# Performance work log

Hardware: AMD Instinct MI355X
Metric: run time of the kernel (lower is better)

The kernel has to match this reference:

```python
import jax, jax.numpy as jnp
import numpy as np

S = 64          # image_size / sdf cube side / embed dim
P = 4           # frame & sdf patch size
NC = 4          # number_of_couples
HP = 8          # num_heads
E = 32          # embedding_middle_attention
FC = 4          # final_number_of_channels
G = S // P      # 16 patches per side
N_FR = G * G * NC      # 1024 frame tokens
N_SDF = G ** 3         # 4096 sdf tokens
N = N_FR + N_SDF       # 5120 total tokens
NB = N // S            # 80 blocks


def setup_inputs() -> dict:
    key = jax.random.key(0)
    ks = jax.random.split(key, 12)
    s = 0.05  # keep attention logits numerically sane
    return {
        "cond1": jax.random.normal(ks[0], (1, 1, S, S, S), jnp.float32),
        "cond2": jax.random.uniform(ks[1], (1, 1, 4 * NC, S, S), jnp.float32),
        "W_emb": jax.random.normal(ks[2], (S, P * P * 4), jnp.float32) * s,   # Linear weight (out,in)
        "b_emb": jnp.zeros((S,), jnp.float32),
        "W_conv3d": jax.random.normal(ks[3], (S, 1, P, P, P), jnp.float32) * s,
        "b_conv3d": jnp.zeros((S,), jnp.float32),
        "pos_emb": jax.random.normal(ks[4], (N, S), jnp.float32) * s,
        "WQ": jax.random.normal(ks[5], (HP, S, E), jnp.float32) * s,
        "WK": jax.random.normal(ks[6], (HP, S, E), jnp.float32) * s,
        "WV": jax.random.normal(ks[7], (HP, S, E), jnp.float32) * s,
        "W_out": jax.random.normal(ks[8], (HP * E, S), jnp.float32) * s,
        "ln_gamma": jnp.ones((N, S), jnp.float32),
        "ln_beta": jnp.zeros((N, S), jnp.float32),
        "W_conv2d": jax.random.normal(ks[9], (S * FC, NB), jnp.float32) * s,  # 1x1 conv (out,in)
        "b_conv2d": jnp.zeros((S * FC,), jnp.float32),
    }


def _frames_to_patches(frames, W_emb, b_emb):
    # frames: (B,1,C,H,W) with C=4*NC, H=W=S
    b = frames.shape[0]
    x = frames[:, 0]                       # (B,C,S,S)
    x = x.transpose(0, 2, 3, 1)            # (B,S,S,C)
    x = x.reshape(b, G, P, G, P, 4 * NC)
    x = x.transpose(0, 1, 3, 2, 4, 5)      # (B,G,G,P,P,C)
    x = x.reshape(b, G * G, P, P, 4 * NC)
    x = x.transpose(0, 1, 4, 2, 3)         # (B,Np,C,P,P)
    # tensor_split along channels into NC chunks, cat along token dim
    x = x.reshape(b, G * G, NC, 4, P, P).transpose(0, 2, 1, 3, 4, 5)
    x = x.reshape(b, N_FR, 4 * P * P)      # flatten (c,i,j) row-major, matches torch
    return x @ W_emb.T + b_emb             # (B, N_FR, S)


def _sdf_to_patches(sdf, W_conv3d, b_conv3d):
    # Conv3d with kernel==stride==P is exact non-overlapping patching + matmul
    b = sdf.shape[0]
    x = sdf[:, 0]                                       # (B,S,S,S)
    x = x.reshape(b, G, P, G, P, G, P)
    x = x.transpose(0, 1, 3, 5, 2, 4, 6)                # (B,G,G,G,P,P,P)
    x = x.reshape(b, N_SDF, P ** 3)
    wc = W_conv3d.reshape(S, P ** 3)                    # (out, d*h*w), same flatten order
    return x @ wc.T + b_conv3d                          # (B, N_SDF, S)


def reference(cond1, cond2, W_emb, b_emb, W_conv3d, b_conv3d, pos_emb,
              WQ, WK, WV, W_out, ln_gamma, ln_beta, W_conv2d, b_conv2d):
    b = cond1.shape[0]
    fr = _frames_to_patches(cond2, W_emb, b_emb)        # (B,1024,64)
    sd = _sdf_to_patches(cond1, W_conv3d, b_conv3d)     # (B,4096,64)
    X = jnp.concatenate([sd, fr], axis=1) + pos_emb     # (B,N,64)

    # manual multi-head attention
    Q = jnp.einsum('bnd,hde->bhne', X, WQ)
    K = jnp.einsum('bnd,hde->bhne', X, WK)
    V = jnp.einsum('bnd,hde->bhne', X, WV)
    scores = jnp.einsum('bhne,bhme->bhnm', Q, K) / jnp.sqrt(jnp.float32(E))
    A = jax.nn.softmax(scores, axis=-1)
    O = jnp.einsum('bhnm,bhme->bhne', A, V)             # (B,H,N,E)
    O = O.transpose(0, 2, 1, 3).reshape(b, N, HP * E)   # head-order concat
    Xn = O @ W_out + X                                  # residual

    # LayerNorm over BOTH (N, emb) axes (torch LayerNorm((N,S)))
    mu = jnp.mean(Xn, axis=(1, 2), keepdims=True)
    var = jnp.mean(jnp.square(Xn - mu), axis=(1, 2), keepdims=True)
    Xn = (Xn - mu) / jnp.sqrt(var + 1e-5) * ln_gamma + ln_beta

    # adapt: reshape to blocks, 1x1 conv2d, reshape to volume
    Xr = Xn.reshape(b, NB, S, S)
    Xc = jnp.einsum('bchw,oc->bohw', Xr, W_conv2d) + b_conv2d[None, :, None, None]
    return Xc.reshape(b, FC, S, S, S)
```

## Files before the change

kernel.cpp:

```cpp
#include <hip/hip_runtime.h>
#include <hip/hip_bf16.h>

typedef short bf16x8 __attribute__((ext_vector_type(8)));
typedef float f32x4 __attribute__((ext_vector_type(4)));
typedef unsigned short u16;
typedef unsigned int u32;

#define NTOK 5120
#define NSDF 4096

__device__ __forceinline__ float b2f(u16 x){
  u32 u = ((u32)x) << 16; float f; __builtin_memcpy(&f, &u, 4); return f;
}
__device__ __forceinline__ u16 f2b(float f){
  u32 u; __builtin_memcpy(&u, &f, 4);
  return (u16)((u + 0x7fffu + ((u >> 16) & 1u)) >> 16);
}
__device__ __forceinline__ u32 cvtpk(float lo, float hi){
  u32 r;
  asm("v_cvt_pk_bf16_f32 %0, %1, %2" : "=v"(r) : "v"(lo), "v"(hi));
  return r;
}
__device__ __forceinline__ f32x4 mfma16(bf16x8 a, bf16x8 b, f32x4 c){
  return __builtin_amdgcn_mfma_f32_16x16x32_bf16(a, b, c, 0, 0, 0);
}
__device__ __forceinline__ void gld16(const void* g, void* l){
  __builtin_amdgcn_global_load_lds(
      (const __attribute__((address_space(1))) u32*)g,
      (__attribute__((address_space(3))) u32*)l, 16, 0, 0);
}

__global__ __launch_bounds__(256) void k_prep(
    const float* __restrict__ WQ, const float* __restrict__ WK, const float* __restrict__ WV,
    const float* __restrict__ W_out, const float* __restrict__ W_emb,
    const float* __restrict__ W_c3, const float* __restrict__ Wc,
    u16* __restrict__ Wt, u16* __restrict__ Wto, u16* __restrict__ Wemb_b,
    u16* __restrict__ Wc3_b, u16* __restrict__ Wcb)
{
  int gid = blockIdx.x * 256 + threadIdx.x;
  int gsz = gridDim.x * 256;
  for (int i = gid; i < 49152; i += gsz){
    int m = i >> 14, r = i & 16383;
    int h = r >> 11, d = (r >> 5) & 63, e = r & 31;
    const float* src = (m == 0) ? WQ : ((m == 1) ? WK : WV);
    float v = src[(h * 64 + d) * 32 + e];
    if (m == 0) v *= 0.17677669529663689f * 1.4426950408889634f;
    Wt[((m * 8 + h) * 32 + e) * 64 + d] = f2b(v);
  }
  for (int i = gid; i < 16384; i += gsz){
    int k = i >> 6, d = i & 63;
    Wto[d * 256 + k] = f2b(W_out[i]);
  }
  for (int i = gid; i < 4096; i += gsz) Wemb_b[i] = f2b(W_emb[i]);
  for (int i = gid; i < 4096; i += gsz) Wc3_b[i] = f2b(W_c3[i]);
  for (int i = gid; i < 20480; i += gsz) Wcb[i] = f2b(Wc[i]);
}

__global__ __launch_bounds__(256) void k_build_x(
    const float* __restrict__ cond1, const float* __restrict__ cond2,
    const u16* __restrict__ Wemb_b, const float* __restrict__ b_emb,
    const u16* __restrict__ Wc3_b, const float* __restrict__ b_c3,
    const float* __restrict__ pos, u16* __restrict__ Xout)
{
  __shared__ __align__(16) u16 Psh[64][72];
  int b = blockIdx.x, t = threadIdx.x;
  bool sdb = (b < 64);
  {
    int nl = t >> 2, sub = t & 3;
    const float* src = sdb ? cond1 : cond2;
    int nn = sdb ? (b * 64 + nl) : (b * 64 + nl - NSDF);
    int g0 = nn >> 8, g1 = (nn >> 4) & 15, g2 = nn & 15;
    const float* sp = src + (g0 * 4 + sub) * 4096 + g1 * 4 * 64 + g2 * 4;
    for (int p1 = 0; p1 < 4; ++p1){
      float4 v = *(const float4*)(sp + p1 * 64);
      ushort4 o;
      o.x = f2b(v.x); o.y = f2b(v.y); o.z = f2b(v.z); o.w = f2b(v.w);
      *(ushort4*)&Psh[nl][sub * 16 + p1 * 4] = o;
    }
  }
  __syncthreads();
  int w = t >> 6, lane = t & 63, l15 = lane & 15, g = lane >> 4;
  const u16* Wm = sdb ? Wc3_b : Wemb_b;
  const float* bias = sdb ? b_c3 : b_emb;
  bf16x8 a0 = *(const bf16x8*)&Psh[w * 16 + l15][g * 8];
  bf16x8 a1 = *(const bf16x8*)&Psh[w * 16 + l15][32 + g * 8];
  for (int nb = 0; nb < 4; ++nb){
    bf16x8 b0 = *(const bf16x8*)(Wm + (nb * 16 + l15) * 64 + g * 8);
    bf16x8 b1 = *(const bf16x8*)(Wm + (nb * 16 + l15) * 64 + 32 + g * 8);
    f32x4 acc = {0.f, 0.f, 0.f, 0.f};
    acc = mfma16(a0, b0, acc);
    acc = mfma16(a1, b1, acc);
    int d = nb * 16 + l15;
    float bs = bias[d];
    for (int r = 0; r < 4; ++r){
      int tok = b * 64 + w * 16 + g * 4 + r;
      float v = acc[r] + bs + pos[tok * 64 + d];
      Xout[tok * 64 + d] = f2b(v);
    }
  }
}

__global__ __launch_bounds__(256) void k_qkv(
    const u16* __restrict__ X, const u16* __restrict__ Wt,
    u16* __restrict__ Q, u16* __restrict__ K, u16* __restrict__ VT)
{
  __shared__ __align__(16) u16 Xsh[64][72];
  int bid = blockIdx.x, b = bid / 6, grp = bid % 6;
  int t = threadIdx.x;
  {
    int nl = t >> 2, cb = t & 3;
    const u16* sp = X + (b * 64 + nl) * 64 + cb * 16;
    *(bf16x8*)&Xsh[nl][cb * 16] = *(const bf16x8*)(sp);
    *(bf16x8*)&Xsh[nl][cb * 16 + 8] = *(const bf16x8*)(sp + 8);
  }
  __syncthreads();
  int w = t >> 6, lane = t & 63, l15 = lane & 15, g = lane >> 4;
  int pair = grp * 4 + w, m = pair >> 3, h = pair & 7;
  bf16x8 a0[4], a1[4];
  for (int ms = 0; ms < 4; ++ms){
    a0[ms] = *(const bf16x8*)&Xsh[ms * 16 + l15][g * 8];
    a1[ms] = *(const bf16x8*)&Xsh[ms * 16 + l15][32 + g * 8];
  }
  for (int nb = 0; nb < 2; ++nb){
    const u16* wp = Wt + ((m * 8 + h) * 32 + nb * 16 + l15) * 64;
    bf16x8 b0 = *(const bf16x8*)(wp + g * 8);
    bf16x8 b1 = *(const bf16x8*)(wp + 32 + g * 8);
    int e = nb * 16 + l15;
    for (int ms = 0; ms < 4; ++ms){
      f32x4 acc = {0.f, 0.f, 0.f, 0.f};
      acc = mfma16(a0[ms], b0, acc);
      acc = mfma16(a1[ms], b1, acc);
      for (int r = 0; r < 4; ++r){
        int n = b * 64 + ms * 16 + g * 4 + r;
        u16 v = f2b(acc[r]);
        if (m == 0)      Q[(h * NTOK + n) * 32 + e] = v;
        else if (m == 1) K[(h * NTOK + n) * 32 + e] = v;
        else             VT[(h * 32 + e) * NTOK + n] = v;
      }
    }
  }
}

__global__ __launch_bounds__(256) void k_attn(
    const u16* __restrict__ Q, const u16* __restrict__ K, const u16* __restrict__ VT,
    u16* __restrict__ Opb, float* __restrict__ lpart)
{
  __shared__ __align__(16) u16 Ksh[2][128 * 32];
  __shared__ __align__(16) u16 Vsh[2][32 * 128];
  int bid = blockIdx.x;
  int x = bid & 7;
  int inner = bid >> 3;
  int qb = inner % 40;
  int p = x + 8 * (inner / 40);
  int sp = p >> 3, h = p & 7;
  int t = threadIdx.x, w = t >> 6, lane = t & 63, l15 = lane & 15, g = lane >> 4;
  int q0w = qb * 128 + w * 32;
  int kb = sp * 1280;
  int wb = w * 512;

  int rho0 = t >> 2, cpK = t & 3;
  int key0 = (rho0 & 0x60) | ((rho0 & 0x0C) << 1) | ((rho0 & 0x10) >> 2) | (rho0 & 3);
  int clogK = cpK ^ (rho0 & 3);
  const uint4* kg0 = (const uint4*)(K + (size_t)(h * NTOK + kb + key0) * 32 + clogK * 8);
  const uint4* kg1 = (const uint4*)(K + (size_t)(h * NTOK + kb + key0 + 64) * 32 + clogK * 8);
  int eV = t >> 4, cpV = t & 15;
  int clogV = cpV ^ eV;
  const uint4* vg0 = (const uint4*)(VT + (size_t)(h * 32 + eV) * NTOK + kb + clogV * 8);
  const uint4* vg1 = (const uint4*)(VT + (size_t)(h * 32 + eV + 16) * NTOK + kb + clogV * 8);

  bf16x8 qf0 = *(const bf16x8*)(Q + (size_t)(h * NTOK + q0w + l15) * 32 + g * 8);
  bf16x8 qf1 = *(const bf16x8*)(Q + (size_t)(h * NTOK + q0w + 16 + l15) * 32 + g * 8);

  f32x4 oc[2][2];
  for (int u = 0; u < 2; ++u) for (int eb = 0; eb < 2; ++eb) oc[u][eb] = (f32x4){0.f,0.f,0.f,0.f};
  float ls0 = 0.f, ls1 = 0.f;

  int kf_base = l15 * 32 + ((g ^ (l15 & 3)) * 8);

  gld16(kg0, &Ksh[0][wb]);
  gld16(kg1, &Ksh[0][wb + 2048]);
  gld16(vg0, &Vsh[0][wb]);
  gld16(vg1, &Vsh[0][wb + 2048]);
  __syncthreads();

  for (int kt = 0; kt < 10; ++kt){
    int cur = kt & 1, nxt = cur ^ 1;
    if (kt < 9){
      gld16(kg0 + (kt + 1) * 512, &Ksh[nxt][wb]);
      gld16(kg1 + (kt + 1) * 512, &Ksh[nxt][wb + 2048]);
      gld16(vg0 + (kt + 1) * 16,  &Vsh[nxt][wb]);
      gld16(vg1 + (kt + 1) * 16,  &Vsh[nxt][wb + 2048]);
    }
    const u16* kB = &Ksh[cur][0];
    const u16* vB = &Vsh[cur][0];
    #pragma unroll
    for (int ks = 0; ks < 4; ++ks){
      f32x4 z = {0.f,0.f,0.f,0.f};
      bf16x8 kf0 = *(const bf16x8*)(kB + kf_base + ks * 1024);
      bf16x8 kf1 = *(const bf16x8*)(kB + kf_base + ks * 1024 + 512);
      f32x4 s0a = mfma16(kf0, qf0, z);
      f32x4 s1a = mfma16(kf1, qf0, z);
      f32x4 s0b = mfma16(kf0, qf1, z);
      f32x4 s1b = mfma16(kf1, qf1, z);
      int vf_off = l15 * 128 + (((ks * 4 + g) ^ l15) * 8);
      bf16x8 vf0 = *(const bf16x8*)(vB + vf_off);
      bf16x8 vf1 = *(const bf16x8*)(vB + vf_off + 2048);
      float pa0 = __builtin_amdgcn_exp2f(s0a[0]);
      float pa1 = __builtin_amdgcn_exp2f(s0a[1]);
      float pa2 = __builtin_amdgcn_exp2f(s0a[2]);
      float pa3 = __builtin_amdgcn_exp2f(s0a[3]);
      float pa4 = __builtin_amdgcn_exp2f(s1a[0]);
      float pa5 = __builtin_amdgcn_exp2f(s1a[1]);
      float pa6 = __builtin_amdgcn_exp2f(s1a[2]);
      float pa7 = __builtin_amdgcn_exp2f(s1a[3]);
      ls0 += ((pa0 + pa1) + (pa2 + pa3)) + ((pa4 + pa5) + (pa6 + pa7));
      union { bf16x8 v; u32 wd[4]; } pua;
      pua.wd[0] = cvtpk(pa0, pa1); pua.wd[1] = cvtpk(pa2, pa3);
      pua.wd[2] = cvtpk(pa4, pa5); pua.wd[3] = cvtpk(pa6, pa7);
      float pb0 = __builtin_amdgcn_exp2f(s0b[0]);
      float pb1 = __builtin_amdgcn_exp2f(s0b[1]);
      float pb2 = __builtin_amdgcn_exp2f(s0b[2]);
      float pb3 = __builtin_amdgcn_exp2f(s0b[3]);
      float pb4 = __builtin_amdgcn_exp2f(s1b[0]);
      float pb5 = __builtin_amdgcn_exp2f(s1b[1]);
      float pb6 = __builtin_amdgcn_exp2f(s1b[2]);
      float pb7 = __builtin_amdgcn_exp2f(s1b[3]);
      ls1 += ((pb0 + pb1) + (pb2 + pb3)) + ((pb4 + pb5) + (pb6 + pb7));
      union { bf16x8 v; u32 wd[4]; } pub;
      pub.wd[0] = cvtpk(pb0, pb1); pub.wd[1] = cvtpk(pb2, pb3);
      pub.wd[2] = cvtpk(pb4, pb5); pub.wd[3] = cvtpk(pb6, pb7);
      oc[0][0] = mfma16(pua.v, vf0, oc[0][0]);
      oc[0][1] = mfma16(pua.v, vf1, oc[0][1]);
      oc[1][0] = mfma16(pub.v, vf0, oc[1][0]);
      oc[1][1] = mfma16(pub.v, vf1, oc[1][1]);
    }
    __syncthreads();
  }

  ls0 += __shfl_xor(ls0, 16); ls0 += __shfl_xor(ls0, 32);
  ls1 += __shfl_xor(ls1, 16); ls1 += __shfl_xor(ls1, 32);

  u16* opp = Opb + ((size_t)(sp * 8 + h) * NTOK + q0w) * 32;
  for (int u = 0; u < 2; ++u)
    for (int eb = 0; eb < 2; ++eb)
      for (int r = 0; r < 4; ++r)
        opp[(u * 16 + 4 * g + r) * 32 + eb * 16 + l15] = f2b(oc[u][eb][r]);
  if (lane < 16){
    lpart[(size_t)(sp * 8 + h) * NTOK + q0w + l15] = ls0;
    lpart[(size_t)(sp * 8 + h) * NTOK + q0w + 16 + l15] = ls1;
  }
}

__global__ __launch_bounds__(256) void k_omerge(
    const u16* __restrict__ Opb, const float* __restrict__ lpart, u16* __restrict__ O)
{
  int gid = blockIdx.x * 256 + threadIdx.x;
  int n = gid >> 5, r = gid & 31, h = r >> 2, eo = r & 3;
  float acc[8] = {0.f,0.f,0.f,0.f,0.f,0.f,0.f,0.f};
  float l = 0.f;
  #pragma unroll
  for (int sp = 0; sp < 4; ++sp){
    union { bf16x8 v; u16 s[8]; } u;
    u.v = *(const bf16x8*)(Opb + (((size_t)(sp * 8 + h) * NTOK + n) << 5) + eo * 8);
    #pragma unroll
    for (int j = 0; j < 8; ++j) acc[j] += b2f(u.s[j]);
    l += lpart[(size_t)(sp * 8 + h) * NTOK + n];
  }
  float rl = 1.0f / l;
  union { bf16x8 v; u32 wd[4]; } o;
  #pragma unroll
  for (int j = 0; j < 4; ++j) o.wd[j] = cvtpk(acc[2*j] * rl, acc[2*j+1] * rl);
  *(bf16x8*)(O + n * 256 + h * 32 + eo * 8) = o.v;
}

__global__ __launch_bounds__(64) void k_xn(
    const u16* __restrict__ O, const u16* __restrict__ Wto,
    const u16* __restrict__ X, float* __restrict__ Xn, float* __restrict__ partials)
{
  int b = blockIdx.x, lane = threadIdx.x, l15 = lane & 15, g = lane >> 4;
  int n0 = b * 16;
  int n = n0 + l15;
  f32x4 acc[4];
  #pragma unroll
  for (int nb = 0; nb < 4; ++nb) acc[nb] = (f32x4){0.f,0.f,0.f,0.f};
  #pragma unroll
  for (int ks = 0; ks < 8; ++ks){
    bf16x8 av = *(const bf16x8*)(O + (size_t)n * 256 + ks * 32 + g * 8);
    #pragma unroll
    for (int nb = 0; nb < 4; ++nb){
      bf16x8 bb = *(const bf16x8*)(Wto + (nb * 16 + l15) * 256 + ks * 32 + g * 8);
      acc[nb] = mfma16(av, bb, acc[nb]);
    }
  }
  float s1 = 0.f, s2 = 0.f;
  #pragma unroll
  for (int nb = 0; nb < 4; ++nb){
    int d = nb * 16 + l15;
    #pragma unroll
    for (int r = 0; r < 4; ++r){
      int nn = n0 + g * 4 + r;
      float v = acc[nb][r] + b2f(X[nn * 64 + d]);
      Xn[nn * 64 + d] = v;
      s1 += v; s2 += v * v;
    }
  }
  for (int off = 1; off < 64; off <<= 1){
    s1 += __shfl_xor(s1, off);
    s2 += __shfl_xor(s2, off);
  }
  if (lane == 0){
    partials[b * 2]     = s1;
    partials[b * 2 + 1] = s2;
  }
}

__global__ __launch_bounds__(256) void k_out(
    const float* __restrict__ Xn, const float* __restrict__ partials,
    const float* __restrict__ gamma, const float* __restrict__ beta,
    const u16* __restrict__ Wcb, const float* __restrict__ bc,
    float* __restrict__ out)
{
  __shared__ float redA[8];
  __shared__ float murs2[2];
  __shared__ __align__(16) float Xs[80 * 16];
  int bid = blockIdx.x, t = threadIdx.x, w = t >> 6, lane = t & 63;
  int hh = bid >> 2, wq = (bid & 3) * 16;
  float s1 = 0.f, s2 = 0.f;
  for (int i = t; i < 320; i += 256){
    s1 += partials[2 * i];
    s2 += partials[2 * i + 1];
  }
  for (int off = 1; off < 64; off <<= 1){ s1 += __shfl_xor(s1, off); s2 += __shfl_xor(s2, off); }
  if (lane == 0){ redA[w * 2] = s1; redA[w * 2 + 1] = s2; }
  __syncthreads();
  if (t == 0){
    float S1 = redA[0] + redA[2] + redA[4] + redA[6];
    float S2 = redA[1] + redA[3] + redA[5] + redA[7];
    const float inv = 1.0f / 327680.0f;
    float mu = S1 * inv;
    murs2[0] = mu;
    murs2[1] = rsqrtf(S2 * inv - mu * mu + 1e-5f);
  }
  __syncthreads();
  float mu = murs2[0], rs = murs2[1];
  for (int i = t; i < 1280; i += 256){
    int c = i >> 4, ww = wq + (i & 15);
    int idx = (c * 64 + hh) * 64 + ww;
    Xs[i] = (Xn[idx] - mu) * rs * gamma[idx] + beta[idx];
  }
  __syncthreads();
  int o = t;
  const u16* wr = Wcb + o * 80;
  f32x4 acc4[4];
  for (int k = 0; k < 4; ++k) acc4[k] = (f32x4){0.f,0.f,0.f,0.f};
  for (int c = 0; c < 80; ++c){
    float wt = b2f(wr[c]);
    for (int k = 0; k < 4; ++k)
      acc4[k] += (*(const f32x4*)&Xs[c * 16 + k * 4]) * wt;
  }
  float bb = bc[o];
  for (int k = 0; k < 4; ++k)
    for (int j = 0; j < 4; ++j)
      out[o * 4096 + hh * 64 + wq + k * 4 + j] = acc4[k][j] + bb;
}

extern "C" void kernel_launch(void* const* d_in, const int* in_sizes, int n_in,
                              void* d_out, int out_size, void* d_ws, size_t ws_size,
                              hipStream_t stream) {
  const float* cond1 = (const float*)d_in[0];
  const float* cond2 = (const float*)d_in[1];
  const float* W_emb = (const float*)d_in[2];
  const float* b_emb = (const float*)d_in[3];
  const float* W_c3  = (const float*)d_in[4];
  const float* b_c3  = (const float*)d_in[5];
  const float* pos   = (const float*)d_in[6];
  const float* WQ    = (const float*)d_in[7];
  const float* WK    = (const float*)d_in[8];
  const float* WV    = (const float*)d_in[9];
  const float* W_out = (const float*)d_in[10];
  const float* gamma = (const float*)d_in[11];
  const float* beta  = (const float*)d_in[12];
  const float* Wc    = (const float*)d_in[13];
  const float* bc    = (const float*)d_in[14];
  float* out = (float*)d_out;
  char* ws = (char*)d_ws;

  u16*   X   = (u16*)(ws);
  u16*   Q   = (u16*)(ws +   655360);
  u16*   Kq  = (u16*)(ws +  3276800);
  u16*   VT  = (u16*)(ws +  5898240);
  u16*   O   = (u16*)(ws +  8519680);
  float* Xn  = (float*)(ws + 11141120);
  u16*   Wt  = (u16*)(ws + 12451840);
  u16*   Wto = (u16*)(ws + 12550144);
  float* partials = (float*)(ws + 12582912);
  u16*   Wemb_b = (u16*)(ws + 12585472);
  u16*   Wc3_b  = (u16*)(ws + 12593664);
  u16*   Wcb    = (u16*)(ws + 12601856);
  u16*   Opb    = (u16*)(ws + 12648448);
  float* lpart  = (float*)(ws + 23134208);

  k_prep<<<32, 256, 0, stream>>>(WQ, WK, WV, W_out, W_emb, W_c3, Wc,
                                 Wt, Wto, Wemb_b, Wc3_b, Wcb);
  k_build_x<<<80, 256, 0, stream>>>(cond1, cond2, Wemb_b, b_emb, Wc3_b, b_c3, pos, X);
  k_qkv<<<480, 256, 0, stream>>>(X, Wt, Q, Kq, VT);
  k_attn<<<1280, 256, 0, stream>>>(Q, Kq, VT, Opb, lpart);
  k_omerge<<<640, 256, 0, stream>>>(Opb, lpart, O);
  k_xn<<<320, 64, 0, stream>>>(O, Wto, X, Xn, partials);
  k_out<<<256, 256, 0, stream>>>(Xn, partials, gamma, beta, Wcb, bc, out);
}
```

Before: 85.00 us.

## Compute softmax row sums via MFMA and use explicit vmcnt waits with raw barriers

The scalar accumulation of exponentiated scores and its cross-lane shuffle reduction are replaced with MFMA products of the bf16 probability fragments against a ones vector, so row sums come out of the matrix unit. The __syncthreads calls are replaced with explicit s_waitcnt vmcnt counts plus raw s_barrier and sched_barrier. This lets the next tile's global-to-LDS loads stay in flight while the current tile is consumed. Risks: sums now use bf16-rounded probabilities, and the hand-written waitcnt is correct only if the count of outstanding loads matches exactly.

```diff
diff --git a/kernel.cpp b/kernel.cpp
--- a/kernel.cpp
+++ b/kernel.cpp
@@ -171,9 +171,14 @@
   bf16x8 qf0 = *(const bf16x8*)(Q + (size_t)(h * NTOK + q0w + l15) * 32 + g * 8);
   bf16x8 qf1 = *(const bf16x8*)(Q + (size_t)(h * NTOK + q0w + 16 + l15) * 32 + g * 8);
 
+  union { u16 s[8]; bf16x8 v; } one8;
+  #pragma unroll
+  for (int j = 0; j < 8; ++j) one8.s[j] = 0x3F80;
+  bf16x8 ones = one8.v;
+
   f32x4 oc[2][2];
   for (int u = 0; u < 2; ++u) for (int eb = 0; eb < 2; ++eb) oc[u][eb] = (f32x4){0.f,0.f,0.f,0.f};
-  float ls0 = 0.f, ls1 = 0.f;
+  f32x4 als0 = {0.f,0.f,0.f,0.f}, als1 = {0.f,0.f,0.f,0.f};
 
   int kf_base = l15 * 32 + ((g ^ (l15 & 3)) * 8);
 
@@ -181,7 +186,6 @@
   gld16(kg1, &Ksh[0][wb + 2048]);
   gld16(vg0, &Vsh[0][wb]);
   gld16(vg1, &Vsh[0][wb + 2048]);
-  __syncthreads();
 
   for (int kt = 0; kt < 10; ++kt){
     int cur = kt & 1, nxt = cur ^ 1;
@@ -190,7 +194,13 @@
       gld16(kg1 + (kt + 1) * 512, &Ksh[nxt][wb + 2048]);
       gld16(vg0 + (kt + 1) * 16,  &Vsh[nxt][wb]);
       gld16(vg1 + (kt + 1) * 16,  &Vsh[nxt][wb + 2048]);
-    }
+      asm volatile("s_waitcnt vmcnt(4)" ::: "memory");
+    } else {
+      asm volatile("s_waitcnt vmcnt(0)" ::: "memory");
+    }
+    __builtin_amdgcn_sched_barrier(0);
+    __builtin_amdgcn_s_barrier();
+    __builtin_amdgcn_sched_barrier(0);
     const u16* kB = &Ksh[cur][0];
     const u16* vB = &Vsh[cur][0];
     #pragma unroll
@@ -213,7 +223,6 @@
       float pa5 = __builtin_amdgcn_exp2f(s1a[1]);
       float pa6 = __builtin_amdgcn_exp2f(s1a[2]);
       float pa7 = __builtin_amdgcn_exp2f(s1a[3]);
-      ls0 += ((pa0 + pa1) + (pa2 + pa3)) + ((pa4 + pa5) + (pa6 + pa7));
       union { bf16x8 v; u32 wd[4]; } pua;
       pua.wd[0] = cvtpk(pa0, pa1); pua.wd[1] = cvtpk(pa2, pa3);
       pua.wd[2] = cvtpk(pa4, pa5); pua.wd[3] = cvtpk(pa6, pa7);
@@ -225,7 +234,6 @@
       float pb5 = __builtin_amdgcn_exp2f(s1b[1]);
       float pb6 = __builtin_amdgcn_exp2f(s1b[2]);
       float pb7 = __builtin_amdgcn_exp2f(s1b[3]);
-      ls1 += ((pb0 + pb1) + (pb2 + pb3)) + ((pb4 + pb5) + (pb6 + pb7));
       union { bf16x8 v; u32 wd[4]; } pub;
       pub.wd[0] = cvtpk(pb0, pb1); pub.wd[1] = cvtpk(pb2, pb3);
       pub.wd[2] = cvtpk(pb4, pb5); pub.wd[3] = cvtpk(pb6, pb7);
@@ -233,21 +241,25 @@
       oc[0][1] = mfma16(pua.v, vf1, oc[0][1]);
       oc[1][0] = mfma16(pub.v, vf0, oc[1][0]);
       oc[1][1] = mfma16(pub.v, vf1, oc[1][1]);
-    }
-    __syncthreads();
-  }
-
-  ls0 += __shfl_xor(ls0, 16); ls0 += __shfl_xor(ls0, 32);
-  ls1 += __shfl_xor(ls1, 16); ls1 += __shfl_xor(ls1, 32);
+      als0 = mfma16(pua.v, ones, als0);
+      als1 = mfma16(pub.v, ones, als1);
+    }
+    __builtin_amdgcn_sched_barrier(0);
+    __builtin_amdgcn_s_barrier();
+  }
 
   u16* opp = Opb + ((size_t)(sp * 8 + h) * NTOK + q0w) * 32;
   for (int u = 0; u < 2; ++u)
     for (int eb = 0; eb < 2; ++eb)
       for (int r = 0; r < 4; ++r)
         opp[(u * 16 + 4 * g + r) * 32 + eb * 16 + l15] = f2b(oc[u][eb][r]);
-  if (lane < 16){
-    lpart[(size_t)(sp * 8 + h) * NTOK + q0w + l15] = ls0;
-    lpart[(size_t)(sp * 8 + h) * NTOK + q0w + 16 + l15] = ls1;
+  if (l15 == 0){
+    float* lp = lpart + (size_t)(sp * 8 + h) * NTOK + q0w;
+    #pragma unroll
+    for (int r = 0; r < 4; ++r){
+      lp[4 * g + r]      = als0[r];
+      lp[16 + 4 * g + r] = als1[r];
+    }
   }
 }
 
```

Result: faster. 82.02 us (-3.5%).
